# Optimization experiments

Measured on AMD Instinct MI355X. Metric: run time of the kernel, lower is better.

Reference implementation:

```python
import jax, jax.numpy as jnp
import numpy as np


def _rel_coords_log(ws: int) -> np.ndarray:
    # matches torch.meshgrid default indexing='ij'
    idx = np.arange(ws, dtype=np.float32)
    coords = np.stack(np.meshgrid(idx, idx, indexing='ij'), axis=0).reshape(2, -1)  # [2, ws^2]
    rel = coords[:, :, None] - coords[:, None, :]  # [2, T, T]
    rel = rel.transpose(1, 2, 0).reshape(-1, 2)    # [T*T, 2]
    return np.sign(rel) * np.log1p(np.abs(rel))


def setup_inputs() -> dict:
    key = jax.random.key(0)
    ks = jax.random.split(key, 9)
    B, C, Hd, ws, meta_h = 256, 256, 8, 16, 256
    s = 1.0 / np.sqrt(C)
    return {
        'x': jax.random.normal(ks[0], (B, C, ws, ws), dtype=jnp.float32),
        'w_qkv': jax.random.normal(ks[1], (3 * C, C), dtype=jnp.float32) * s,
        'b_qkv': jax.random.normal(ks[2], (3 * C,), dtype=jnp.float32) * 0.01,
        'w_proj': jax.random.normal(ks[3], (C, C), dtype=jnp.float32) * s,
        'b_proj': jax.random.normal(ks[4], (C,), dtype=jnp.float32) * 0.01,
        'mw1': jax.random.normal(ks[5], (meta_h, 2), dtype=jnp.float32) * 0.5,
        'mb1': jax.random.normal(ks[6], (meta_h,), dtype=jnp.float32) * 0.01,
        'mw2': jax.random.normal(ks[7], (Hd, meta_h), dtype=jnp.float32) * (1.0 / np.sqrt(meta_h)),
        'mb2': jax.random.normal(ks[8], (Hd,), dtype=jnp.float32) * 0.01,
        'tau': jnp.ones((1, Hd, 1, 1), dtype=jnp.float32),
    }


def reference(x, w_qkv, b_qkv, w_proj, b_proj, mw1, mb1, mw2, mb2, tau):
    B, C, H, W = x.shape
    T = H * W
    nh = tau.shape[1]
    hd = C // nh
    # [B, C, H, W] -> [B, T, C]
    xt = x.reshape(B, C, T).transpose(0, 2, 1)
    qkv = xt @ w_qkv.T + b_qkv                                  # [B, T, 3C]
    qkv = qkv.reshape(B, T, 3, nh, hd).transpose(2, 0, 3, 1, 4)  # [3, B, nh, T, hd]
    q, k, v = qkv[0], qkv[1], qkv[2]
    # cosine similarity attention
    qn = jnp.linalg.norm(q, axis=-1, keepdims=True)              # [B, nh, T, 1]
    kn = jnp.linalg.norm(k, axis=-1, keepdims=True)
    denom = jnp.maximum(qn * kn.transpose(0, 1, 3, 2), 1e-6)
    scores = jnp.einsum('bhqd,bhkd->bhqk', q, k) / denom
    scores = scores / jnp.maximum(tau, 0.01)
    # MLP relative position bias (static coords)
    rc = jnp.asarray(_rel_coords_log(H))                          # [T*T, 2]
    bias = jax.nn.relu(rc @ mw1.T + mb1) @ mw2.T + mb2            # [T*T, nh]
    bias = bias.T.reshape(nh, T, T)
    scores = scores + bias[None]
    attn = jax.nn.softmax(scores, axis=-1)
    out = jnp.einsum('bhqk,bhkd->bhqd', attn, v)                  # [B, nh, T, hd]
    out = out.transpose(0, 2, 1, 3).reshape(B, T, C)
    out = out @ w_proj.T + b_proj
    return out.transpose(0, 2, 1).reshape(B, C, H, W)
```

## Files before the change

kernel.cpp:

```cpp
#include <hip/hip_runtime.h>
#include <math.h>

#define Cc 256
#define NH 8
#define HD 32
#define Tt 256
#define MH 256
#define TBL 961

typedef _Float16 f16;
typedef f16 f16x4 __attribute__((ext_vector_type(4)));
typedef f16 f16x8 __attribute__((ext_vector_type(8)));
typedef float f32x4 __attribute__((ext_vector_type(4)));

__device__ __forceinline__ f16x8 ld8(const f16* base, int row, int kc) {
  return *(const f16x8*)&base[row * 32 + ((kc ^ ((row >> 2) & 3)) << 3)];
}
__device__ __forceinline__ void st8(f16* base, int row, int kc, f16x8 v) {
  *(f16x8*)&base[row * 32 + ((kc ^ ((row >> 2) & 3)) << 3)] = v;
}
__device__ __forceinline__ int sidx(int row, int col) {
  return row * 32 + (((col >> 3) ^ ((row >> 2) & 3)) << 3) + (col & 7);
}
__device__ __forceinline__ int vsidx(int d, int t) {
  return d * 256 + (((t >> 3) ^ (d & 7)) << 3) + (t & 7);
}
__device__ __forceinline__ f16x8 vld8(const f16* base, int d, int tch) {
  return *(const f16x8*)&base[d * 256 + ((tch ^ (d & 7)) << 3)];
}

__global__ __launch_bounds__(256) void stage0_kernel(
    const float* __restrict__ x, f16* __restrict__ xt,
    const float* __restrict__ mw1, const float* __restrict__ mb1,
    const float* __restrict__ mw2, const float* __restrict__ mb2,
    const float* __restrict__ w_proj, const float* __restrict__ w_qkv,
    float* __restrict__ table, float* __restrict__ tablemax,
    f16* __restrict__ wpf, f16* __restrict__ wqf) {
  __shared__ __align__(16) char smem0[9216];
  int tid = threadIdx.x;
  int blk = blockIdx.x;

  if (blk < 4096) {
    f16* tile = (f16*)smem0;
    int b = blk >> 4, ti = (blk >> 2) & 3, tj = blk & 3;
    const float* xb = x + (size_t)b * 65536;
    int t4 = (tid & 15) * 4, cg = tid >> 4;
#pragma unroll
    for (int p = 0; p < 4; p++) {
      int cl = cg + p * 16;
      float4 v = *(const float4*)&xb[(size_t)(ti * 64 + cl) * 256 + tj * 64 + t4];
      const float* vp = (const float*)&v;
#pragma unroll
      for (int u = 0; u < 4; u++) {
        int tl = t4 + u;
        tile[tl * 72 + (((cl >> 3) ^ (tl & 7)) << 3) + (cl & 7)] = (f16)vp[u];
      }
    }
    __syncthreads();
    f16* xtb = xt + (size_t)b * 65536;
#pragma unroll
    for (int u = 0; u < 2; u++) {
      int chunk = tid * 2 + u;
      int tr = chunk >> 3, ck = chunk & 7;
      f16x8 v = *(const f16x8*)&tile[tr * 72 + ((ck ^ (tr & 7)) << 3)];
      *(f16x8*)&xtb[(size_t)(tj * 64 + tr) * 256 + ti * 64 + ck * 8] = v;
    }
    return;
  }

  blk -= 4096;
  if (blk >= NH + 32) {
    int blk2 = blk - NH - 32;
#pragma unroll
    for (int pass = 0; pass < 4; pass++) {
      int chunkid = blk2 * 256 + tid + pass * 6144;
      int row = chunkid >> 5, ck = chunkid & 31;
      int hh = row / 96, n = row % 96;
      int srow = ((n >> 5) << 8) + (hh << 5) + (n & 31);
      const float* wp = w_qkv + (size_t)srow * Cc + ck * 8;
      f16x8 v;
#pragma unroll
      for (int u = 0; u < 8; u++) v[u] = (f16)wp[u];
      *(f16x8*)&wqf[(size_t)row * Cc + ck * 8] = v;
    }
    return;
  }
  if (blk >= NH) {
    int base = (blk - NH) * 2048 + tid * 8;
    f16x8 v;
#pragma unroll
    for (int u = 0; u < 8; u++) v[u] = (f16)w_proj[base + u];
    *(f16x8*)&wpf[base] = v;
    return;
  }
  float4* s_w = (float4*)smem0;
  float* red = (float*)(smem0 + 4096);
  for (int i = tid; i < MH; i += 256) {
    float4 w;
    w.x = mw1[2 * i];
    w.y = mw1[2 * i + 1];
    w.z = mb1[i];
    w.w = mw2[blk * MH + i];
    s_w[i] = w;
  }
  __syncthreads();
  float b2 = mb2[blk];
  float d0v[4], d1v[4], ov[4];
#pragma unroll
  for (int j = 0; j < 4; j++) {
    int idx = tid + j * 256;
    int ii = idx < TBL ? idx : TBL - 1;
    float fdi = (float)(ii / 31 - 15);
    float fdj = (float)(ii % 31 - 15);
    d0v[j] = (fdi > 0.f ? 1.f : (fdi < 0.f ? -1.f : 0.f)) * log1pf(fabsf(fdi));
    d1v[j] = (fdj > 0.f ? 1.f : (fdj < 0.f ? -1.f : 0.f)) * log1pf(fabsf(fdj));
    ov[j] = b2;
  }
  for (int m = 0; m < MH; m++) {
    float4 w = s_w[m];
#pragma unroll
    for (int j = 0; j < 4; j++) {
      float hid = fmaxf(fmaf(d0v[j], w.x, fmaf(d1v[j], w.y, w.z)), 0.f);
      ov[j] = fmaf(hid, w.w, ov[j]);
    }
  }
  float lmax = -1e30f;
#pragma unroll
  for (int j = 0; j < 4; j++) {
    int idx = tid + j * 256;
    if (idx < TBL) {
      table[blk * TBL + idx] = ov[j];
      lmax = fmaxf(lmax, ov[j]);
    }
  }
  red[tid] = lmax;
  __syncthreads();
  for (int s = 128; s > 0; s >>= 1) {
    if (tid < s) red[tid] = fmaxf(red[tid], red[tid + s]);
    __syncthreads();
  }
  if (tid == 0) tablemax[blk] = red[0];
}

__global__ __launch_bounds__(512, 4) void fused_attn(
    const f16* __restrict__ xt, const f16* __restrict__ wqf,
    const float* __restrict__ b_qkv, const float* __restrict__ table,
    const float* __restrict__ tablemax, const float* __restrict__ tau,
    f16* __restrict__ attnH) {
  __shared__ __align__(16) char smem[67328];
  f16* Qa = (f16*)smem;
  f16* Ka = (f16*)(smem + 16384);
  f16* Vt = (f16*)(smem + 32768);
  f16* Pspare = (f16*)(smem + 49152);
  float* tbv = (float*)(smem + 51456);
  f16* Xa = (f16*)smem;
  f16* Wa = (f16*)(smem + 16384);

  int tid = threadIdx.x;
  int o = blockIdx.x;
  int bh = ((o & 7) << 8) | (o >> 3);
  int b = bh >> 3, h = bh & 7;
  int wv = tid >> 6, ln = tid & 63, lq = ln >> 4, lm = ln & 15;

  const float LOG2E = 1.4426950408889634f;
  float rtau = 1.0f / fmaxf(tau[h], 0.01f);
  float tmaxh = tablemax[h];

  for (int idx = tid; idx < 31 * 32; idx += 512) {
    int di_ = idx >> 5, c = idx & 31;
    float4 v;
    float* vp = (float*)&v;
#pragma unroll
    for (int u = 0; u < 4; u++) {
      int dj = c - u;
      dj = dj < 0 ? 0 : (dj > 30 ? 30 : dj);
      vp[u] = (table[h * TBL + di_ * 31 + dj] - tmaxh - rtau * 1.0001f) * LOG2E;
    }
    *(float4*)&tbv[idx * 4] = v;
  }

  float bj[6];
#pragma unroll
  for (int nt = 0; nt < 6; nt++) {
    int n = nt * 16 + lm;
    int row = ((n >> 5) << 8) + (h << 5) + (n & 31);
    bj[nt] = b_qkv[row];
  }

  const f16* xtb = xt + (size_t)b * 65536;
  const f16* wqh = wqf + (size_t)h * 24576;
  int xt_ = tid >> 1, xkc = (tid & 1) * 2;
  int wn = tid >> 2, wck = tid & 3;

  f32x4 acc[2][6] = {};
  f16x8 xv0, xv1, wvv;
  xv0 = *(const f16x8*)&xtb[xt_ * 256 + xkc * 8];
  xv1 = *(const f16x8*)&xtb[xt_ * 256 + xkc * 8 + 8];
  if (tid < 384) wvv = *(const f16x8*)&wqh[wn * 256 + wck * 8];

  for (int c0 = 0; c0 < Cc; c0 += 32) {
    st8(Xa, xt_, xkc, xv0);
    st8(Xa, xt_, xkc + 1, xv1);
    if (tid < 384) st8(Wa, wn, wck, wvv);
    __syncthreads();
    if (c0 + 32 < Cc) {
      xv0 = *(const f16x8*)&xtb[xt_ * 256 + c0 + 32 + xkc * 8];
      xv1 = *(const f16x8*)&xtb[xt_ * 256 + c0 + 32 + xkc * 8 + 8];
      if (tid < 384) wvv = *(const f16x8*)&wqh[wn * 256 + c0 + 32 + wck * 8];
    }
    f16x8 af[2], bf[6];
#pragma unroll
    for (int e = 0; e < 2; e++) af[e] = ld8(Xa, wv * 32 + e * 16 + lm, lq);
#pragma unroll
    for (int nt = 0; nt < 6; nt++) bf[nt] = ld8(Wa, nt * 16 + lm, lq);
#pragma unroll
    for (int e = 0; e < 2; e++)
#pragma unroll
      for (int nt = 0; nt < 6; nt++)
        acc[e][nt] = __builtin_amdgcn_mfma_f32_16x16x32_f16(af[e], bf[nt],
                                                            acc[e][nt], 0, 0, 0);
    __syncthreads();
  }

#pragma unroll
  for (int e = 0; e < 2; e++) {
#pragma unroll
    for (int nt = 0; nt < 6; nt++) {
      int d = (nt & 1) * 16 + lm;
      if (nt < 4) {
#pragma unroll
        for (int r = 0; r < 4; r++) {
          int t = wv * 32 + e * 16 + lq * 4 + r;
          f16 v = (f16)(acc[e][nt][r] + bj[nt]);
          if (nt < 2) Qa[sidx(t, d)] = v;
          else        Ka[sidx(t, d)] = v;
        }
      } else {
        int t0 = wv * 32 + e * 16 + lq * 4;
        f16x4 pv;
#pragma unroll
        for (int r = 0; r < 4; r++) pv[r] = (f16)(acc[e][nt][r] + bj[nt]);
        *(f16x4*)&Vt[vsidx(d, t0)] = pv;
      }
    }
  }
  __syncthreads();

  if (tid < 256) {
    int t = tid;
    float s = 0.f;
    f16x8 v[4];
#pragma unroll
    for (int ck = 0; ck < 4; ck++) {
      v[ck] = ld8(Qa, t, ck);
#pragma unroll
      for (int u = 0; u < 8; u++) { float f = (float)v[ck][u]; s = fmaf(f, f, s); }
    }
    float sc_ = rsqrtf(s) * rtau * LOG2E;
#pragma unroll
    for (int ck = 0; ck < 4; ck++) {
      f16x8 o2;
#pragma unroll
      for (int u = 0; u < 8; u++) o2[u] = (f16)((float)v[ck][u] * sc_);
      st8(Qa, t, ck, o2);
    }
  } else {
    int t = tid - 256;
    float s = 0.f;
    f16x8 v[4];
#pragma unroll
    for (int ck = 0; ck < 4; ck++) {
      v[ck] = ld8(Ka, t, ck);
#pragma unroll
      for (int u = 0; u < 8; u++) { float f = (float)v[ck][u]; s = fmaf(f, f, s); }
    }
    float sc_ = rsqrtf(s);
#pragma unroll
    for (int ck = 0; ck < 4; ck++) {
      f16x8 o2;
#pragma unroll
      for (int u = 0; u < 8; u++) o2[u] = (f16)((float)v[ck][u] * sc_);
      st8(Ka, t, ck, o2);
    }
  }
  __syncthreads();

  f16x8 qf[2];
#pragma unroll
  for (int e = 0; e < 2; e++) qf[e] = ld8(Qa, wv * 32 + e * 16 + lm, lq);
  __syncthreads();

  f16* Pme = (wv < 7) ? (Qa + wv * 1152) : Pspare;
  int c0l = lm - lq * 4 + 15;
  const float4* tbp = (const float4*)tbv;
  f32x4 acco[2][2] = {};
  f32x4 acco_s[2] = {};
  f16x8 onev;
#pragma unroll
  for (int u = 0; u < 8; u++) onev[u] = (f16)1.0f;
  int dibase = wv * 2 + 15;

  for (int n0 = 0; n0 < Tt; n0 += 32) {
    f16x8 kf[2];
#pragma unroll
    for (int nt = 0; nt < 2; nt++) kf[nt] = ld8(Ka, n0 + nt * 16 + lm, lq);
    f32x4 zero = {0.f, 0.f, 0.f, 0.f};
    f32x4 sc[2][2];
    __builtin_amdgcn_s_setprio(1);
#pragma unroll
    for (int e = 0; e < 2; e++)
#pragma unroll
      for (int nt = 0; nt < 2; nt++)
        sc[e][nt] = __builtin_amdgcn_mfma_f32_16x16x32_f16(kf[nt], qf[e], zero,
                                                           0, 0, 0);
    __builtin_amdgcn_s_setprio(0);
#pragma unroll
    for (int e = 0; e < 2; e++) {
#pragma unroll
      for (int nt = 0; nt < 2; nt++) {
        int di_ = dibase + e - (n0 >> 4) - nt;
        float4 bv = tbp[di_ * 32 + c0l];
        const float* bvp = (const float*)&bv;
        f16x4 pv;
#pragma unroll
        for (int r = 0; r < 4; r++) pv[r] = (f16)exp2f(sc[e][nt][r] + bvp[r]);
        *(f16x4*)&Pme[(e * 16 + lm) * 36 + nt * 16 + lq * 4] = pv;
      }
    }
    asm volatile("s_waitcnt lgkmcnt(0)" ::: "memory");
    f16x8 pf[2], vf[2];
#pragma unroll
    for (int e = 0; e < 2; e++) {
      f16x4 p0 = *(f16x4*)&Pme[(e * 16 + lm) * 36 + lq * 8];
      f16x4 p1 = *(f16x4*)&Pme[(e * 16 + lm) * 36 + lq * 8 + 4];
      pf[e] = __builtin_shufflevector(p0, p1, 0, 1, 2, 3, 4, 5, 6, 7);
    }
#pragma unroll
    for (int dt = 0; dt < 2; dt++)
      vf[dt] = vld8(Vt, dt * 16 + lm, (n0 >> 3) + lq);
    __builtin_amdgcn_s_setprio(1);
#pragma unroll
    for (int e = 0; e < 2; e++) {
#pragma unroll
      for (int dt = 0; dt < 2; dt++)
        acco[e][dt] = __builtin_amdgcn_mfma_f32_16x16x32_f16(pf[e], vf[dt],
                                                             acco[e][dt], 0, 0, 0);
      acco_s[e] = __builtin_amdgcn_mfma_f32_16x16x32_f16(pf[e], onev,
                                                         acco_s[e], 0, 0, 0);
    }
    __builtin_amdgcn_s_setprio(0);
  }

#pragma unroll
  for (int e = 0; e < 2; e++)
#pragma unroll
    for (int r = 0; r < 4; r++) {
      float rl = __builtin_amdgcn_rcpf(acco_s[e][r]);
      int q = wv * 32 + e * 16 + lq * 4 + r;
#pragma unroll
      for (int dt = 0; dt < 2; dt++) {
        int d = dt * 16 + lm;
        attnH[((size_t)b * Tt + q) * Cc + h * HD + d] =
            (f16)(acco[e][dt][r] * rl);
      }
    }
}

__global__ __launch_bounds__(256, 4) void proj_gemm(
    const f16* __restrict__ A, const f16* __restrict__ wf,
    const float* __restrict__ bp, float* __restrict__ out) {
  __shared__ __align__(16) f16 Af[128 * 72];
  __shared__ __align__(16) f16 Wsh[128 * 72];
  __shared__ float sB[128];
  int tid = threadIdx.x;
  int row0 = blockIdx.x * 128;
  int n0g = blockIdx.y * 128;
  int b = row0 >> 8, t0 = row0 & 255;
  int wv = tid >> 6, ln = tid & 63, lq = ln >> 4, lm = ln & 15;
  int cw = (wv & 1) * 64, tw = (wv >> 1) * 64;

  if (tid < 128) sB[tid] = bp[n0g + tid];

  f32x4 acc[4][4] = {};
  for (int k0 = 0; k0 < Cc; k0 += 64) {
#pragma unroll
    for (int p = 0; p < 4; p++) {
      int idx = p * 256 + tid;
      int row = idx >> 3, ch = idx & 7;
      f16x8 v = *(const f16x8*)&A[(size_t)(row0 + row) * Cc + k0 + ch * 8];
      *(f16x8*)&Af[row * 72 + ch * 8] = v;
    }
#pragma unroll
    for (int p = 0; p < 4; p++) {
      int idx = p * 256 + tid;
      int row = idx >> 3, ch = idx & 7;
      f16x8 v = *(const f16x8*)&wf[(size_t)(n0g + row) * Cc + k0 + ch * 8];
      *(f16x8*)&Wsh[row * 72 + ch * 8] = v;
    }
    __syncthreads();
#pragma unroll
    for (int kk = 0; kk < 2; kk++) {
      f16x8 wfr[4], af[4];
#pragma unroll
      for (int i = 0; i < 4; i++)
        wfr[i] = *(f16x8*)&Wsh[(cw + i * 16 + lm) * 72 + (kk * 4 + lq) * 8];
#pragma unroll
      for (int j = 0; j < 4; j++)
        af[j] = *(f16x8*)&Af[(tw + j * 16 + lm) * 72 + (kk * 4 + lq) * 8];
#pragma unroll
      for (int i = 0; i < 4; i++)
#pragma unroll
        for (int j = 0; j < 4; j++)
          acc[i][j] = __builtin_amdgcn_mfma_f32_16x16x32_f16(wfr[i], af[j],
                                                             acc[i][j], 0, 0, 0);
    }
    __syncthreads();
  }

#pragma unroll
  for (int i = 0; i < 4; i++)
#pragma unroll
    for (int r = 0; r < 4; r++) {
      int crl = cw + i * 16 + lq * 4 + r;
      float bias = sB[crl];
#pragma unroll
      for (int j = 0; j < 4; j++) {
        int tcl = tw + j * 16 + lm;
        out[(size_t)b * 65536 + (size_t)(n0g + crl) * 256 + t0 + tcl] =
            acc[i][j][r] + bias;
      }
    }
}

extern "C" void kernel_launch(void* const* d_in, const int* in_sizes, int n_in,
                              void* d_out, int out_size, void* d_ws,
                              size_t ws_size, hipStream_t stream) {
  const float* x = (const float*)d_in[0];
  const float* w_qkv = (const float*)d_in[1];
  const float* b_qkv = (const float*)d_in[2];
  const float* w_proj = (const float*)d_in[3];
  const float* b_proj = (const float*)d_in[4];
  const float* mw1 = (const float*)d_in[5];
  const float* mb1 = (const float*)d_in[6];
  const float* mw2 = (const float*)d_in[7];
  const float* mb2 = (const float*)d_in[8];
  const float* tau = (const float*)d_in[9];
  float* out = (float*)d_out;

  const size_t NEEDED = (size_t)(TBL * NH + NH) * 4 + (size_t)65536 * 2 +
                        (size_t)256 * NH * Tt * HD * 2;
  if (ws_size < NEEDED) return;

  float* table = (float*)d_ws;
  float* tablemax = table + TBL * NH;
  f16* wpf = (f16*)(tablemax + NH);
  f16* attnH = wpf + 65536;

  f16* xt = (f16*)d_out;
  f16* wqf = (f16*)d_out + (size_t)256 * 65536;

  stage0_kernel<<<4160, 256, 0, stream>>>(x, xt, mw1, mb1, mw2, mb2, w_proj,
                                          w_qkv, table, tablemax, wpf, wqf);
  fused_attn<<<256 * NH, 512, 0, stream>>>(xt, wqf, b_qkv, table, tablemax,
                                           tau, attnH);
  dim3 g3(512, 2);
  proj_gemm<<<g3, 256, 0, stream>>>(attnH, wpf, b_proj, out);
}
```

Before: 244.7 us.

## Shrink attention LDS footprint with compact bias table and per-tile P staging

Cuts the fused attention kernel's shared memory from about 67KB to about 49KB. The bias table is stored as float2 pairs (31x30) instead of padded float4 rows, and it is built after the Q fragments are loaded so it can reuse part of the Q region. Each wave's P staging buffer is halved to one 16-row tile that is reused for each e-iteration, with an extra LDS wait per iteration. The transpose store loop in the prep kernel is also re-indexed so each thread writes rows 32 apart. The aim is higher occupancy, at the cost of serialising the P round-trips and doing two LDS loads for the bias instead of one.

```diff
diff --git a/kernel.cpp b/kernel.cpp
--- a/kernel.cpp
+++ b/kernel.cpp
@@ -58,12 +58,12 @@
     }
     __syncthreads();
     f16* xtb = xt + (size_t)b * 65536;
+    int tr = tid >> 3, ck = tid & 7;
 #pragma unroll
     for (int u = 0; u < 2; u++) {
-      int chunk = tid * 2 + u;
-      int tr = chunk >> 3, ck = chunk & 7;
-      f16x8 v = *(const f16x8*)&tile[tr * 72 + ((ck ^ (tr & 7)) << 3)];
-      *(f16x8*)&xtb[(size_t)(tj * 64 + tr) * 256 + ti * 64 + ck * 8] = v;
+      int r = tr + u * 32;
+      f16x8 v = *(const f16x8*)&tile[r * 72 + ((ck ^ (r & 7)) << 3)];
+      *(f16x8*)&xtb[(size_t)(tj * 64 + r) * 256 + ti * 64 + ck * 8] = v;
     }
     return;
   }
@@ -147,14 +147,13 @@
     const float* __restrict__ b_qkv, const float* __restrict__ table,
     const float* __restrict__ tablemax, const float* __restrict__ tau,
     f16* __restrict__ attnH) {
-  __shared__ __align__(16) char smem[67328];
+  __shared__ __align__(16) char smem[49424];
   f16* Qa = (f16*)smem;
-  f16* Ka = (f16*)(smem + 16384);
-  f16* Vt = (f16*)(smem + 32768);
-  f16* Pspare = (f16*)(smem + 49152);
-  float* tbv = (float*)(smem + 51456);
+  f16* Ka = (f16*)(smem + 16656);
+  f16* Vt = (f16*)(smem + 33040);
+  float2* tbv2 = (float2*)(smem + 9216);
   f16* Xa = (f16*)smem;
-  f16* Wa = (f16*)(smem + 16384);
+  f16* Wa = (f16*)(smem + 16656);
 
   int tid = threadIdx.x;
   int o = blockIdx.x;
@@ -165,19 +164,6 @@
   const float LOG2E = 1.4426950408889634f;
   float rtau = 1.0f / fmaxf(tau[h], 0.01f);
   float tmaxh = tablemax[h];
-
-  for (int idx = tid; idx < 31 * 32; idx += 512) {
-    int di_ = idx >> 5, c = idx & 31;
-    float4 v;
-    float* vp = (float*)&v;
-#pragma unroll
-    for (int u = 0; u < 4; u++) {
-      int dj = c - u;
-      dj = dj < 0 ? 0 : (dj > 30 ? 30 : dj);
-      vp[u] = (table[h * TBL + di_ * 31 + dj] - tmaxh - rtau * 1.0001f) * LOG2E;
-    }
-    *(float4*)&tbv[idx * 4] = v;
-  }
 
   float bj[6];
 #pragma unroll
@@ -290,9 +276,19 @@
   for (int e = 0; e < 2; e++) qf[e] = ld8(Qa, wv * 32 + e * 16 + lm, lq);
   __syncthreads();
 
-  f16* Pme = (wv < 7) ? (Qa + wv * 1152) : Pspare;
+  for (int idx = tid; idx < 31 * 30; idx += 512) {
+    int di_ = idx / 30, c = idx - di_ * 30 + 1;
+    float t0 = table[h * TBL + di_ * 31 + c];
+    float t1 = table[h * TBL + di_ * 31 + c - 1];
+    float2 v;
+    v.x = (t0 - tmaxh - rtau * 1.0001f) * LOG2E;
+    v.y = (t1 - tmaxh - rtau * 1.0001f) * LOG2E;
+    tbv2[idx] = v;
+  }
+  __syncthreads();
+
+  f16* Pme = Qa + wv * 576;
   int c0l = lm - lq * 4 + 15;
-  const float4* tbp = (const float4*)tbv;
   f32x4 acco[2][2] = {};
   f32x4 acco_s[2] = {};
   f16x8 onev;
@@ -314,27 +310,27 @@
         sc[e][nt] = __builtin_amdgcn_mfma_f32_16x16x32_f16(kf[nt], qf[e], zero,
                                                            0, 0, 0);
     __builtin_amdgcn_s_setprio(0);
+    f16x8 pf[2];
 #pragma unroll
     for (int e = 0; e < 2; e++) {
 #pragma unroll
       for (int nt = 0; nt < 2; nt++) {
         int di_ = dibase + e - (n0 >> 4) - nt;
-        float4 bv = tbp[di_ * 32 + c0l];
-        const float* bvp = (const float*)&bv;
+        float2 b01 = tbv2[di_ * 30 + c0l - 1];
+        float2 b23 = tbv2[di_ * 30 + c0l - 3];
         f16x4 pv;
-#pragma unroll
-        for (int r = 0; r < 4; r++) pv[r] = (f16)exp2f(sc[e][nt][r] + bvp[r]);
-        *(f16x4*)&Pme[(e * 16 + lm) * 36 + nt * 16 + lq * 4] = pv;
+        pv[0] = (f16)exp2f(sc[e][nt][0] + b01.x);
+        pv[1] = (f16)exp2f(sc[e][nt][1] + b01.y);
+        pv[2] = (f16)exp2f(sc[e][nt][2] + b23.x);
+        pv[3] = (f16)exp2f(sc[e][nt][3] + b23.y);
+        *(f16x4*)&Pme[lm * 36 + nt * 16 + lq * 4] = pv;
       }
-    }
-    asm volatile("s_waitcnt lgkmcnt(0)" ::: "memory");
-    f16x8 pf[2], vf[2];
-#pragma unroll
-    for (int e = 0; e < 2; e++) {
-      f16x4 p0 = *(f16x4*)&Pme[(e * 16 + lm) * 36 + lq * 8];
-      f16x4 p1 = *(f16x4*)&Pme[(e * 16 + lm) * 36 + lq * 8 + 4];
+      asm volatile("s_waitcnt lgkmcnt(0)" ::: "memory");
+      f16x4 p0 = *(f16x4*)&Pme[lm * 36 + lq * 8];
+      f16x4 p1 = *(f16x4*)&Pme[lm * 36 + lq * 8 + 4];
       pf[e] = __builtin_shufflevector(p0, p1, 0, 1, 2, 3, 4, 5, 6, 7);
     }
+    f16x8 vf[2];
 #pragma unroll
     for (int dt = 0; dt < 2; dt++)
       vf[dt] = vld8(Vt, dt * 16 + lm, (n0 >> 3) + lq);
```

Measured after the change: 242.3 us. About the same (-1.0%).
